# Kernel optimization log

Hardware: AMD Instinct MI355X
Metric: run time of the kernel (lower is better)

The kernel has to match this reference:

```python
import jax, jax.numpy as jnp
import numpy as np

IN_F, OUT_F = 128, 128
B, N = 4, 4096

def setup_inputs() -> dict:
    key = jax.random.key(0)
    k1, k2, k3 = jax.random.split(key, 3)
    relation_matrix = jax.random.uniform(k1, (B, N, N), dtype=jnp.float32)
    inputs = jax.random.normal(k2, (B, N, IN_F), dtype=jnp.float32)
    w = jax.random.normal(k3, (IN_F, OUT_F), dtype=jnp.float32)
    return {"relation_matrix": relation_matrix, "inputs": inputs, "w": w}

def reference(relation_matrix, inputs, w):
    # deg_i = sum_j A_ij ; D = diag(deg) + I  -> inverse is elementwise reciprocal
    deg = jnp.sum(relation_matrix, axis=-1) + 1.0            # [B, N]
    # (A + I) @ X  == A @ X + X  (avoids materializing A + eye)
    ax = jnp.einsum('bnm,bmf->bnf', relation_matrix, inputs) + inputs  # [B, N, in]
    z = (ax / deg[..., None]) @ w                            # [B, N, out]
    return jax.nn.relu(z)
```

## Files before the change

### kernel.cpp

```cpp
#include <hip/hip_runtime.h>
#include <hip/hip_bf16.h>
#include <stdint.h>

#define NN 4096
#define NF 128
#define NBATCH 4

typedef __attribute__((ext_vector_type(4))) float  floatx4;
typedef __attribute__((ext_vector_type(8))) __bf16 bf16x8;

__global__ __launch_bounds__(256) void prep_kernel(const float* __restrict__ X,
                                                   const float* __restrict__ w,
                                                   __bf16* __restrict__ XT,
                                                   __bf16* __restrict__ wT) {
    int bx = blockIdx.x;
    if (bx == 1024) {
        for (int i = threadIdx.x; i < NF * NF; i += 256) {
            int n = i >> 7, k = i & 127;
            wT[i] = (__bf16)w[k * NF + n];
        }
        return;
    }
    int id  = bx * 256 + threadIdx.x;
    int b   = id >> 16;
    int rem = id & 65535;
    int kc  = rem >> 7;
    int n   = rem & 127;
    const float* Xp = X + (size_t)b * NN * NF + (size_t)kc * 8 * NF + n;
    bf16x8 v;
#pragma unroll
    for (int i = 0; i < 8; i++) v[i] = (__bf16)Xp[(size_t)i * NF];
    *(bf16x8*)(XT + (size_t)b * NF * NN + (size_t)n * NN + kc * 8) = v;
}

__global__ __launch_bounds__(256, 1) void main_kernel(const float* __restrict__ A,
                                                      const float* __restrict__ X,
                                                      const __bf16* __restrict__ XT,
                                                      const __bf16* __restrict__ wT,
                                                      float* __restrict__ out) {
    __shared__ __bf16 Us[64][136];
    __shared__ __bf16 wTs[128][136];
    __shared__ float  degs[64];

    const int tid  = threadIdx.x;
    const int wv   = tid >> 6;
    const int lane = tid & 63;
    const int lm   = lane & 15;
    const int quad = lane >> 4;

    const int bx = blockIdx.x;
    const int b  = bx >> 6;
    const int m0 = (bx & 63) * 64;

    for (int i = tid; i < NF * NF; i += 256)
        wTs[i >> 7][i & 127] = wT[i];

    const int row = m0 + wv * 16 + lm;
    const float*  Arow = A  + ((size_t)b * NN + row) * NN + quad * 8;
    const __bf16* XTb  = XT + (size_t)b * NF * NN + (size_t)lm * NN + quad * 8;

    floatx4 acc[8];
#pragma unroll
    for (int t = 0; t < 8; t++) acc[t] = (floatx4){0.f, 0.f, 0.f, 0.f};
    float dsum = 0.f;

    floatx4 a0 = *(const floatx4*)(Arow);
    floatx4 a1 = *(const floatx4*)(Arow + 4);
    bf16x8 bfr[8];
#pragma unroll
    for (int nt = 0; nt < 8; nt++)
        bfr[nt] = *(const bf16x8*)(XTb + (size_t)nt * 16 * NN);

#pragma unroll 2
    for (int k0 = 0; k0 < NN; k0 += 32) {
        floatx4 na0, na1;
        bf16x8  nb[8];
        if (k0 + 32 < NN) {
            const float* Ap = Arow + k0 + 32;
            na0 = *(const floatx4*)(Ap);
            na1 = *(const floatx4*)(Ap + 4);
            const __bf16* Bp = XTb + k0 + 32;
#pragma unroll
            for (int nt = 0; nt < 8; nt++)
                nb[nt] = *(const bf16x8*)(Bp + (size_t)nt * 16 * NN);
        }
        dsum += a0[0] + a0[1] + a0[2] + a0[3] + a1[0] + a1[1] + a1[2] + a1[3];
        bf16x8 af;
#pragma unroll
        for (int i = 0; i < 4; i++) af[i] = (__bf16)a0[i];
#pragma unroll
        for (int i = 0; i < 4; i++) af[4 + i] = (__bf16)a1[i];
#pragma unroll
        for (int nt = 0; nt < 8; nt++)
            acc[nt] = __builtin_amdgcn_mfma_f32_16x16x32_bf16(af, bfr[nt], acc[nt], 0, 0, 0);
        a0 = na0; a1 = na1;
#pragma unroll
        for (int nt = 0; nt < 8; nt++) bfr[nt] = nb[nt];
    }

    dsum += __shfl_xor(dsum, 16, 64);
    dsum += __shfl_xor(dsum, 32, 64);
    if (lane < 16) degs[wv * 16 + lm] = dsum + 1.0f;
    __syncthreads();

    const float* Xb = X + ((size_t)b * NN + m0) * NF;
#pragma unroll
    for (int nt = 0; nt < 8; nt++) {
        int col = nt * 16 + lm;
#pragma unroll
        for (int i = 0; i < 4; i++) {
            int r = wv * 16 + quad * 4 + i;
            float u = (acc[nt][i] + Xb[(size_t)r * NF + col]) / degs[r];
            Us[r][col] = (__bf16)u;
        }
    }
    __syncthreads();

    floatx4 z[8];
#pragma unroll
    for (int t = 0; t < 8; t++) z[t] = (floatx4){0.f, 0.f, 0.f, 0.f};
#pragma unroll
    for (int kk = 0; kk < NF; kk += 32) {
        bf16x8 ua = *(const bf16x8*)&Us[wv * 16 + lm][kk + quad * 8];
#pragma unroll
        for (int nt = 0; nt < 8; nt++) {
            bf16x8 wb = *(const bf16x8*)&wTs[nt * 16 + lm][kk + quad * 8];
            z[nt] = __builtin_amdgcn_mfma_f32_16x16x32_bf16(ua, wb, z[nt], 0, 0, 0);
        }
    }

    float* ob = out + ((size_t)b * NN + m0) * NF;
#pragma unroll
    for (int nt = 0; nt < 8; nt++) {
        int col = nt * 16 + lm;
#pragma unroll
        for (int i = 0; i < 4; i++) {
            int r = wv * 16 + quad * 4 + i;
            float v = z[nt][i];
            ob[(size_t)r * NF + col] = v > 0.f ? v : 0.f;
        }
    }
}

extern "C" void kernel_launch(void* const* d_in, const int* in_sizes, int n_in,
                              void* d_out, int out_size, void* d_ws, size_t ws_size,
                              hipStream_t stream) {
    const float* A = (const float*)d_in[0];
    const float* X = (const float*)d_in[1];
    const float* w = (const float*)d_in[2];
    float* out = (float*)d_out;

    __bf16* XT = (__bf16*)d_ws;
    __bf16* wT = XT + (size_t)NBATCH * NF * NN;

    prep_kernel<<<1025, 256, 0, stream>>>(X, w, XT, wT);
    main_kernel<<<256, 256, 0, stream>>>(A, X, XT, wT, out);
}
```

Before: 466.8 us.

## Split work into 16-row blocks with per-wave column slices and packed operand layout

```diff
diff --git a/kernel.cpp b/kernel.cpp
--- a/kernel.cpp
+++ b/kernel.cpp
@@ -4,43 +4,53 @@
 
 #define NN 4096
 #define NF 128
-#define NBATCH 4
+#define NB 4
 
 typedef __attribute__((ext_vector_type(4))) float  floatx4;
 typedef __attribute__((ext_vector_type(8))) __bf16 bf16x8;
 
 __global__ __launch_bounds__(256) void prep_kernel(const float* __restrict__ X,
                                                    const float* __restrict__ w,
-                                                   __bf16* __restrict__ XT,
-                                                   __bf16* __restrict__ wT) {
-    int bx = blockIdx.x;
-    if (bx == 1024) {
-        for (int i = threadIdx.x; i < NF * NF; i += 256) {
-            int n = i >> 7, k = i & 127;
-            wT[i] = (__bf16)w[k * NF + n];
+                                                   __bf16* __restrict__ Xpack,
+                                                   __bf16* __restrict__ wpack) {
+    const int tid = threadIdx.x;
+    const int bx  = blockIdx.x;
+    if (bx == 256) {
+        for (int p = tid; p < 512; p += 256) {
+            int kc = p >> 7, n = p & 127;
+#pragma unroll
+            for (int k8 = 0; k8 < 32; k8 += 8) {
+                bf16x8 v;
+#pragma unroll
+                for (int j = 0; j < 8; j++)
+                    v[j] = (__bf16)w[(size_t)(kc * 32 + k8 + j) * NF + n];
+                *(bf16x8*)(wpack + ((size_t)(kc * 128 + n)) * 32 + k8) = v;
+            }
         }
         return;
     }
-    int id  = bx * 256 + threadIdx.x;
-    int b   = id >> 16;
-    int rem = id & 65535;
-    int kc  = rem >> 7;
-    int n   = rem & 127;
-    const float* Xp = X + (size_t)b * NN * NF + (size_t)kc * 8 * NF + n;
-    bf16x8 v;
+    int id = bx * 256 + tid;
+    int b  = id >> 14;
+    int kc = (id >> 7) & 127;
+    int n  = id & 127;
+    const float* Xp = X + ((size_t)b * NN + (size_t)kc * 32) * NF + n;
+    __bf16* op = Xpack + (((size_t)b * 128 + kc) * 128 + n) * 32;
 #pragma unroll
-    for (int i = 0; i < 8; i++) v[i] = (__bf16)Xp[(size_t)i * NF];
-    *(bf16x8*)(XT + (size_t)b * NF * NN + (size_t)n * NN + kc * 8) = v;
+    for (int k8 = 0; k8 < 32; k8 += 8) {
+        bf16x8 v;
+#pragma unroll
+        for (int j = 0; j < 8; j++)
+            v[j] = (__bf16)Xp[(size_t)(k8 + j) * NF];
+        *(bf16x8*)(op + k8) = v;
+    }
 }
 
-__global__ __launch_bounds__(256, 1) void main_kernel(const float* __restrict__ A,
+__global__ __launch_bounds__(256, 4) void main_kernel(const float* __restrict__ A,
                                                       const float* __restrict__ X,
-                                                      const __bf16* __restrict__ XT,
-                                                      const __bf16* __restrict__ wT,
+                                                      const __bf16* __restrict__ Xpack,
+                                                      const __bf16* __restrict__ wpack,
                                                       float* __restrict__ out) {
-    __shared__ __bf16 Us[64][136];
-    __shared__ __bf16 wTs[128][136];
-    __shared__ float  degs[64];
+    __shared__ __bf16 Us[16][136];
 
     const int tid  = threadIdx.x;
     const int wv   = tid >> 6;
@@ -48,95 +58,99 @@
     const int lm   = lane & 15;
     const int quad = lane >> 4;
 
-    const int bx = blockIdx.x;
-    const int b  = bx >> 6;
-    const int m0 = (bx & 63) * 64;
+    const int b  = blockIdx.x >> 8;
+    const int m0 = (blockIdx.x & 255) << 4;
 
-    for (int i = tid; i < NF * NF; i += 256)
-        wTs[i >> 7][i & 127] = wT[i];
+    const float*  Arow = A + ((size_t)b * NN + m0 + lm) * NN + quad * 8;
+    const __bf16* Bp   = Xpack + ((size_t)b * 128 * NF + (wv * 32 + lm)) * 32 + quad * 8;
 
-    const int row = m0 + wv * 16 + lm;
-    const float*  Arow = A  + ((size_t)b * NN + row) * NN + quad * 8;
-    const __bf16* XTb  = XT + (size_t)b * NF * NN + (size_t)lm * NN + quad * 8;
-
-    floatx4 acc[8];
-#pragma unroll
-    for (int t = 0; t < 8; t++) acc[t] = (floatx4){0.f, 0.f, 0.f, 0.f};
+    floatx4 acc0 = {0.f, 0.f, 0.f, 0.f};
+    floatx4 acc1 = {0.f, 0.f, 0.f, 0.f};
     float dsum = 0.f;
 
     floatx4 a0 = *(const floatx4*)(Arow);
     floatx4 a1 = *(const floatx4*)(Arow + 4);
-    bf16x8 bfr[8];
-#pragma unroll
-    for (int nt = 0; nt < 8; nt++)
-        bfr[nt] = *(const bf16x8*)(XTb + (size_t)nt * 16 * NN);
+    bf16x8  b0 = *(const bf16x8*)(Bp);
+    bf16x8  b1 = *(const bf16x8*)(Bp + 512);
 
-#pragma unroll 2
-    for (int k0 = 0; k0 < NN; k0 += 32) {
-        floatx4 na0, na1;
-        bf16x8  nb[8];
-        if (k0 + 32 < NN) {
-            const float* Ap = Arow + k0 + 32;
-            na0 = *(const floatx4*)(Ap);
-            na1 = *(const floatx4*)(Ap + 4);
-            const __bf16* Bp = XTb + k0 + 32;
-#pragma unroll
-            for (int nt = 0; nt < 8; nt++)
-                nb[nt] = *(const bf16x8*)(Bp + (size_t)nt * 16 * NN);
-        }
+#pragma unroll 4
+    for (int kc = 0; kc < 127; kc++) {
+        const float*  An = Arow + (size_t)(kc + 1) * 32;
+        const __bf16* Bn = Bp + (size_t)(kc + 1) * 4096;
+        floatx4 na0 = *(const floatx4*)(An);
+        floatx4 na1 = *(const floatx4*)(An + 4);
+        bf16x8  nb0 = *(const bf16x8*)(Bn);
+        bf16x8  nb1 = *(const bf16x8*)(Bn + 512);
+
         dsum += a0[0] + a0[1] + a0[2] + a0[3] + a1[0] + a1[1] + a1[2] + a1[3];
         bf16x8 af;
 #pragma unroll
         for (int i = 0; i < 4; i++) af[i] = (__bf16)a0[i];
 #pragma unroll
         for (int i = 0; i < 4; i++) af[4 + i] = (__bf16)a1[i];
+        acc0 = __builtin_amdgcn_mfma_f32_16x16x32_bf16(af, b0, acc0, 0, 0, 0);
+        acc1 = __builtin_amdgcn_mfma_f32_16x16x32_bf16(af, b1, acc1, 0, 0, 0);
+
+        a0 = na0; a1 = na1; b0 = nb0; b1 = nb1;
+    }
+    {
+        dsum += a0[0] + a0[1] + a0[2] + a0[3] + a1[0] + a1[1] + a1[2] + a1[3];
+        bf16x8 af;
 #pragma unroll
-        for (int nt = 0; nt < 8; nt++)
-            acc[nt] = __builtin_amdgcn_mfma_f32_16x16x32_bf16(af, bfr[nt], acc[nt], 0, 0, 0);
-        a0 = na0; a1 = na1;
+        for (int i = 0; i < 4; i++) af[i] = (__bf16)a0[i];
 #pragma unroll
-        for (int nt = 0; nt < 8; nt++) bfr[nt] = nb[nt];
+        for (int i = 0; i < 4; i++) af[4 + i] = (__bf16)a1[i];
+        acc0 = __builtin_amdgcn_mfma_f32_16x16x32_bf16(af, b0, acc0, 0, 0, 0);
+        acc1 = __builtin_amdgcn_mfma_f32_16x16x32_bf16(af, b1, acc1, 0, 0, 0);
     }
 
     dsum += __shfl_xor(dsum, 16, 64);
     dsum += __shfl_xor(dsum, 32, 64);
-    if (lane < 16) degs[wv * 16 + lm] = dsum + 1.0f;
-    __syncthreads();
+    float degv[4];
+#pragma unroll
+    for (int i = 0; i < 4; i++)
+        degv[i] = __shfl(dsum, quad * 4 + i, 64) + 1.0f;
+
+    bf16x8 wf[4][2];
+#pragma unroll
+    for (int kc2 = 0; kc2 < 4; kc2++)
+#pragma unroll
+        for (int nt = 0; nt < 2; nt++)
+            wf[kc2][nt] = *(const bf16x8*)(wpack +
+                ((size_t)(kc2 * 128 + wv * 32 + nt * 16 + lm)) * 32 + quad * 8);
 
     const float* Xb = X + ((size_t)b * NN + m0) * NF;
 #pragma unroll
-    for (int nt = 0; nt < 8; nt++) {
-        int col = nt * 16 + lm;
+    for (int nt = 0; nt < 2; nt++) {
+        int col = wv * 32 + nt * 16 + lm;
+        floatx4 accv = nt ? acc1 : acc0;
 #pragma unroll
         for (int i = 0; i < 4; i++) {
-            int r = wv * 16 + quad * 4 + i;
-            float u = (acc[nt][i] + Xb[(size_t)r * NF + col]) / degs[r];
+            int r = quad * 4 + i;
+            float u = (accv[i] + Xb[(size_t)r * NF + col]) / degv[i];
             Us[r][col] = (__bf16)u;
         }
     }
     __syncthreads();
 
-    floatx4 z[8];
+    floatx4 z0 = {0.f, 0.f, 0.f, 0.f};
+    floatx4 z1 = {0.f, 0.f, 0.f, 0.f};
 #pragma unroll
-    for (int t = 0; t < 8; t++) z[t] = (floatx4){0.f, 0.f, 0.f, 0.f};
-#pragma unroll
-    for (int kk = 0; kk < NF; kk += 32) {
-        bf16x8 ua = *(const bf16x8*)&Us[wv * 16 + lm][kk + quad * 8];
-#pragma unroll
-        for (int nt = 0; nt < 8; nt++) {
-            bf16x8 wb = *(const bf16x8*)&wTs[nt * 16 + lm][kk + quad * 8];
-            z[nt] = __builtin_amdgcn_mfma_f32_16x16x32_bf16(ua, wb, z[nt], 0, 0, 0);
-        }
+    for (int kc2 = 0; kc2 < 4; kc2++) {
+        bf16x8 ua = *(const bf16x8*)&Us[lm][kc2 * 32 + quad * 8];
+        z0 = __builtin_amdgcn_mfma_f32_16x16x32_bf16(ua, wf[kc2][0], z0, 0, 0, 0);
+        z1 = __builtin_amdgcn_mfma_f32_16x16x32_bf16(ua, wf[kc2][1], z1, 0, 0, 0);
     }
 
     float* ob = out + ((size_t)b * NN + m0) * NF;
 #pragma unroll
-    for (int nt = 0; nt < 8; nt++) {
-        int col = nt * 16 + lm;
+    for (int nt = 0; nt < 2; nt++) {
+        int col = wv * 32 + nt * 16 + lm;
+        floatx4 zv = nt ? z1 : z0;
 #pragma unroll
         for (int i = 0; i < 4; i++) {
-            int r = wv * 16 + quad * 4 + i;
-            float v = z[nt][i];
+            int r = quad * 4 + i;
+            float v = zv[i];
             ob[(size_t)r * NF + col] = v > 0.f ? v : 0.f;
         }
     }
@@ -150,9 +164,9 @@
     const float* w = (const float*)d_in[2];
     float* out = (float*)d_out;
 
-    __bf16* XT = (__bf16*)d_ws;
-    __bf16* wT = XT + (size_t)NBATCH * NF * NN;
+    __bf16* Xpack = (__bf16*)d_ws;
+    __bf16* wpack = Xpack + (size_t)NB * NF * NN;
 
-    prep_kernel<<<1025, 256, 0, stream>>>(X, w, XT, wT);
-    main_kernel<<<256, 256, 0, stream>>>(A, X, XT, wT, out);
+    prep_kernel<<<257, 256, 0, stream>>>(X, w, Xpack, wpack);
+    main_kernel<<<1024, 256, 0, stream>>>(A, X, Xpack, wpack, out);
 }
```

New measurement: 471.6 us. About the same (+1.0%).
